# Kernel tuning notes

Measured on AMD Instinct MI355X. Metric: run time of the kernel, lower is better.

Reference implementation:

```python
import jax, jax.numpy as jnp
import numpy as np

B, S, D = 4, 2048, 1024

def setup_inputs() -> dict:
    key = jax.random.key(0)
    ks = jax.random.split(key, 9)
    sc = 1.0 / np.sqrt(D)
    return {
        "x": jax.random.normal(ks[0], (B, S, D), dtype=jnp.float32),
        "Wq": jax.random.normal(ks[1], (D, D), dtype=jnp.float32) * sc,
        "bq": jnp.zeros((D,), dtype=jnp.float32),
        "Wk": jax.random.normal(ks[2], (D, D), dtype=jnp.float32) * sc,
        "bk": jnp.zeros((D,), dtype=jnp.float32),
        "Wv": jax.random.normal(ks[3], (D, D), dtype=jnp.float32) * sc,
        "bv": jnp.zeros((D,), dtype=jnp.float32),
        "Wo": jax.random.normal(ks[4], (D, D), dtype=jnp.float32) * sc,
        "bo": jnp.zeros((D,), dtype=jnp.float32),
    }

def _gaussian_mask(seq_len, dtype):
    # exp(-0.5*((pos - S/2)/(S/4))^2), shape [1,1,S] -> broadcasts over KEY axis
    pos = jnp.arange(seq_len, dtype=dtype)
    center = seq_len / 2
    sigma = seq_len / 4
    m = jnp.exp(-0.5 * ((pos - center) / sigma) ** 2)
    return m[None, None, :]

def reference(x, Wq, bq, Wk, bk, Wv, bv, Wo, bo):
    d = x.shape[-1]
    Q = x @ Wq.T + bq            # [B,S,D]
    K = x @ Wk.T + bk
    V = x @ Wv.T + bv
    scores = jnp.einsum('bqd,bkd->bqk', Q, K) / jnp.sqrt(jnp.asarray(d, x.dtype))
    scores = scores * _gaussian_mask(x.shape[1], x.dtype)
    attn = jax.nn.softmax(scores, axis=-1)
    out = jnp.einsum('bqk,bkd->bqd', attn, V)
    return out @ Wo.T + bo
```

## Files before the change

### kernel.cpp

```cpp
#include <hip/hip_runtime.h>
#include <math.h>

#define SEQ 2048
#define DIM 1024

typedef __attribute__((ext_vector_type(8))) _Float16 half8;
typedef __attribute__((ext_vector_type(4))) float f32x4;

__device__ __forceinline__ unsigned short f2h(float f) {
    union { _Float16 h; unsigned short u; } c; c.h = (_Float16)f;
    return c.u;
}
__device__ __forceinline__ float gmask(int k) {
    float t = ((float)k - 1024.0f) * (1.0f / 512.0f);
    return expf(-0.5f * t * t);
}
__device__ __forceinline__ void glds16(const unsigned short* gp, unsigned short* lp) {
    __builtin_amdgcn_global_load_lds((const __attribute__((address_space(1))) void*)gp,
                                     (__attribute__((address_space(3))) void*)lp, 16, 0, 0);
}

__device__ __forceinline__ void stage64(const unsigned short* __restrict__ g, int ldK,
                                        unsigned short* lds, int wave, int lane) {
    int row = wave * 32 + (lane >> 3);
    int seg = (lane & 7) ^ (lane >> 3);
    const unsigned short* gp = g + (long)row * ldK + seg * 8;
    unsigned short* lp = lds + wave * 2048;
    glds16(gp, lp);
    glds16(gp + 8 * (long)ldK, lp + 512);
    glds16(gp + 16 * (long)ldK, lp + 1024);
    glds16(gp + 24 * (long)ldK, lp + 1536);
}

enum { EPI_QKV = 0, EPI_EXP = 1, EPI_PV = 2, EPI_OUT = 3 };

template <int EPI>
__global__ __launch_bounds__(256, 4) void mfma_gemm(
    const unsigned short* __restrict__ A, const unsigned short* __restrict__ Bm,
    const float* __restrict__ bias,
    float* __restrict__ Cf, unsigned short* __restrict__ Ch,
    int M, int N, int K, float scale, long sA, long sB, long sC)
{
    __shared__ unsigned short As[128 * 64];
    __shared__ unsigned short Bs[128 * 64];

    const int bz = blockIdx.z;
    const int tid = threadIdx.x;
    const int wave = tid >> 6;
    const int lane = tid & 63;
    const int wm = (wave & 1) * 64;
    const int wn = (wave >> 1) * 64;
    const long m0 = (long)blockIdx.y * 128;
    const long n0 = (long)blockIdx.x * 128;
    const int lm = lane & 15;
    const int lk = lane >> 4;

    const unsigned short* pA = A + bz * sA + m0 * K;
    const unsigned short* pB = Bm + bz * sB + n0 * K;

    f32x4 acc[4][4];
#pragma unroll
    for (int i = 0; i < 4; ++i)
#pragma unroll
        for (int j = 0; j < 4; ++j) {
            acc[i][j].x = 0.f; acc[i][j].y = 0.f; acc[i][j].z = 0.f; acc[i][j].w = 0.f;
        }

    int aoff[4][2], boff[4][2];
#pragma unroll
    for (int i = 0; i < 4; ++i)
#pragma unroll
        for (int t = 0; t < 2; ++t) {
            int ar = wm + i * 16 + lm;
            aoff[i][t] = ar * 64 + (((4 * t + lk) ^ (ar & 7)) << 3);
            int br = wn + i * 16 + lm;
            boff[i][t] = br * 64 + (((4 * t + lk) ^ (br & 7)) << 3);
        }

    const int pr = (wave & 1) * 64 + lane;
    const int ph = wave >> 1;
    float psum = 0.f;

    for (int k0 = 0; k0 < K; k0 += 64) {
        stage64(pA + k0, K, As, wave, lane);
        stage64(pB + k0, K, Bs, wave, lane);
        __syncthreads();

        if (EPI == EPI_PV) {
            const unsigned short* rowp = As + pr * 64;
#pragma unroll
            for (int i2 = 0; i2 < 4; ++i2) {
                half8 h = *(const half8*)(rowp + (((2 * i2 + ph) ^ (pr & 7)) << 3));
#pragma unroll
                for (int e = 0; e < 8; ++e) psum += (float)h[e];
            }
        }

#pragma unroll
        for (int t = 0; t < 2; ++t) {
            half8 a[4], b[4];
#pragma unroll
            for (int i = 0; i < 4; ++i) a[i] = *(const half8*)(As + aoff[i][t]);
#pragma unroll
            for (int j = 0; j < 4; ++j) b[j] = *(const half8*)(Bs + boff[j][t]);
#pragma unroll
            for (int i = 0; i < 4; ++i)
#pragma unroll
                for (int j = 0; j < 4; ++j)
                    acc[i][j] = __builtin_amdgcn_mfma_f32_16x16x32_f16(a[i], b[j], acc[i][j], 0, 0, 0);
        }
        __syncthreads();
    }

    float* rsf = (float*)As;
    if (EPI == EPI_PV) {
        rsf[ph * 128 + pr] = psum;
        __syncthreads();
    }

    const long MD = 8388608;
    float* cF = (EPI == EPI_OUT) ? Cf + bz * sC : (float*)nullptr;
    unsigned short* cH = (EPI != EPI_OUT) ? Ch + bz * sC : (unsigned short*)nullptr;

#pragma unroll
    for (int i = 0; i < 4; ++i) {
        long mrow = m0 + wm + i * 16 + lk * 4;
        int lr = wm + i * 16 + lk * 4;
        float inv4[4];
        if (EPI == EPI_PV) {
#pragma unroll
            for (int r = 0; r < 4; ++r)
                inv4[r] = 1.0f / (rsf[lr + r] + rsf[128 + lr + r]);
        }
#pragma unroll
        for (int j = 0; j < 4; ++j) {
            int n = (int)n0 + wn + j * 16 + lm;
            if (EPI == EPI_QKV) {
                int sel = n >> 10;
                int n1 = n & 1023;
                float bs = bias[n];
                if (sel < 2) {
                    unsigned short* dst = cH + (long)sel * MD;
#pragma unroll
                    for (int r = 0; r < 4; ++r)
                        dst[(mrow + r) * (long)DIM + n1] = f2h(acc[i][j][r] + bs);
                } else {
                    long b = mrow >> 11, s = mrow & 2047;
                    long idx = 2 * MD + b * (long)DIM * SEQ + (long)n1 * SEQ + s;
                    unsigned long long pk =
                        (unsigned long long)f2h(acc[i][j].x + bs) |
                        ((unsigned long long)f2h(acc[i][j].y + bs) << 16) |
                        ((unsigned long long)f2h(acc[i][j].z + bs) << 32) |
                        ((unsigned long long)f2h(acc[i][j].w + bs) << 48);
                    *(unsigned long long*)(cH + idx) = pk;
                }
            } else if (EPI == EPI_EXP) {
                float mult = scale * gmask(n);
#pragma unroll
                for (int r = 0; r < 4; ++r)
                    cH[(mrow + r) * (long)N + n] = f2h(expf(acc[i][j][r] * mult));
            } else if (EPI == EPI_PV) {
#pragma unroll
                for (int r = 0; r < 4; ++r)
                    cH[(mrow + r) * (long)N + n] = f2h(acc[i][j][r] * inv4[r]);
            } else {
                float bs = bias[n];
#pragma unroll
                for (int r = 0; r < 4; ++r)
                    cF[(mrow + r) * (long)N + n] = acc[i][j][r] + bs;
            }
        }
    }
}

__global__ __launch_bounds__(256) void prep(
    const float* __restrict__ x,
    const float* __restrict__ Wq, const float* __restrict__ Wk,
    const float* __restrict__ Wv, const float* __restrict__ Wo,
    const float* __restrict__ b0, const float* __restrict__ b1, const float* __restrict__ b2,
    unsigned short* __restrict__ xh, unsigned short* __restrict__ Wp, float* __restrict__ bqkv)
{
    long gid = (long)blockIdx.x * 256 + threadIdx.x;
    if (gid < 3072) {
        int sel = (int)(gid >> 10);
        const float* s = sel == 0 ? b0 : sel == 1 ? b1 : b2;
        bqkv[gid] = s[gid & 1023];
    }
    const long NX = 8388608 / 4;
    const long NW = 1048576 / 4;
    const long total = NX + 4 * NW;
    for (long i = gid; i < total; i += (long)gridDim.x * 256) {
        const float* src; unsigned short* dst; long off;
        if (i < NX) { src = x; dst = xh; off = i; }
        else {
            long wi = i - NX;
            int sel = (int)(wi >> 18);
            src = sel == 0 ? Wq : sel == 1 ? Wk : sel == 2 ? Wv : Wo;
            dst = Wp + ((long)sel << 20);
            off = wi & (NW - 1);
        }
        float4 v = ((const float4*)src)[off];
        unsigned long long p = (unsigned long long)f2h(v.x) | ((unsigned long long)f2h(v.y) << 16) |
                               ((unsigned long long)f2h(v.z) << 32) | ((unsigned long long)f2h(v.w) << 48);
        ((unsigned long long*)dst)[off] = p;
    }
}

extern "C" void kernel_launch(void* const* d_in, const int* in_sizes, int n_in,
                              void* d_out, int out_size, void* d_ws, size_t ws_size,
                              hipStream_t stream)
{
    const float* x  = (const float*)d_in[0];
    const float* Wq = (const float*)d_in[1];
    const float* bq = (const float*)d_in[2];
    const float* Wk = (const float*)d_in[3];
    const float* bk = (const float*)d_in[4];
    const float* Wv = (const float*)d_in[5];
    const float* bv = (const float*)d_in[6];
    const float* Wo = (const float*)d_in[7];
    const float* bo = (const float*)d_in[8];
    float* out = (float*)d_out;

    const long MD = 4L * SEQ * DIM;
    const long WW = (long)DIM * DIM;
    const long SD = (long)SEQ * DIM, SS = (long)SEQ * SEQ;

    unsigned short* xh   = (unsigned short*)d_ws;
    unsigned short* Wp   = xh + MD;
    unsigned short* Woh  = Wp + 3 * WW;
    float* bqkv          = (float*)(Wp + 4 * WW);
    unsigned short* Qh   = (unsigned short*)(bqkv + 4096);
    unsigned short* VT   = Qh + 2 * MD;
    unsigned short* expS = Qh + 3 * MD;
    unsigned short* O1   = xh;

    dim3 blk(256);
    prep<<<4096, blk, 0, stream>>>(x, Wq, Wk, Wv, Wo, bq, bk, bv, xh, Wp, bqkv);

    mfma_gemm<EPI_QKV><<<dim3(3 * DIM / 128, (4 * SEQ) / 128, 1), blk, 0, stream>>>(
        xh, Wp, bqkv, nullptr, Qh, 4 * SEQ, 3 * DIM, DIM, 1.0f, 0, 0, 0);
    mfma_gemm<EPI_EXP><<<dim3(SEQ / 128, SEQ / 128, 4), blk, 0, stream>>>(
        Qh, Qh + MD, nullptr, nullptr, expS, SEQ, SEQ, DIM, 0.03125f, SD, SD, SS);
    mfma_gemm<EPI_PV><<<dim3(DIM / 128, SEQ / 128, 4), blk, 0, stream>>>(
        expS, VT, nullptr, nullptr, O1, SEQ, DIM, SEQ, 1.0f, SS, (long)DIM * SEQ, SD);
    mfma_gemm<EPI_OUT><<<dim3(DIM / 128, (4 * SEQ) / 128, 1), blk, 0, stream>>>(
        O1, Woh, bo, out, nullptr, 4 * SEQ, DIM, DIM, 1.0f, 0, 0, 0);
}
```

Measured before the change: 277.1 us.

## Fuse all stages into one persistent cooperative kernel with grid syncs

Replaces the five separate launches (conversion, QKV GEMM, score-exp GEMM, PV GEMM, output GEMM) with one persistent cooperative kernel. Blocks loop over tiles for each stage and are separated by grid-wide syncs. The aim is to remove per-launch overhead and the idle gaps between dependent kernels. In exchange it adds grid.sync cost, fixes the grid size to the occupancy-limited count, and gives up any overlap the hardware scheduler could find across kernel boundaries.

```diff
diff --git a/kernel.cpp b/kernel.cpp
--- a/kernel.cpp
+++ b/kernel.cpp
@@ -1,5 +1,8 @@
 #include <hip/hip_runtime.h>
+#include <hip/hip_cooperative_groups.h>
 #include <math.h>
+
+namespace cg = cooperative_groups;
 
 #define SEQ 2048
 #define DIM 1024
@@ -35,23 +38,20 @@
 enum { EPI_QKV = 0, EPI_EXP = 1, EPI_PV = 2, EPI_OUT = 3 };
 
 template <int EPI>
-__global__ __launch_bounds__(256, 4) void mfma_gemm(
+__device__ __forceinline__ void gemm_tile(
+    unsigned short* As, unsigned short* Bs, int tid,
+    int tm, int tn, int bz,
     const unsigned short* __restrict__ A, const unsigned short* __restrict__ Bm,
     const float* __restrict__ bias,
     float* __restrict__ Cf, unsigned short* __restrict__ Ch,
-    int M, int N, int K, float scale, long sA, long sB, long sC)
+    int N, int K, float scale, long sA, long sB, long sC)
 {
-    __shared__ unsigned short As[128 * 64];
-    __shared__ unsigned short Bs[128 * 64];
-
-    const int bz = blockIdx.z;
-    const int tid = threadIdx.x;
     const int wave = tid >> 6;
     const int lane = tid & 63;
     const int wm = (wave & 1) * 64;
     const int wn = (wave >> 1) * 64;
-    const long m0 = (long)blockIdx.y * 128;
-    const long n0 = (long)blockIdx.x * 128;
+    const long m0 = (long)tm * 128;
+    const long n0 = (long)tn * 128;
     const int lm = lane & 15;
     const int lk = lane >> 4;
 
@@ -173,37 +173,81 @@
     }
 }
 
-__global__ __launch_bounds__(256) void prep(
+__global__ __launch_bounds__(256, 4) void mega(
     const float* __restrict__ x,
-    const float* __restrict__ Wq, const float* __restrict__ Wk,
-    const float* __restrict__ Wv, const float* __restrict__ Wo,
-    const float* __restrict__ b0, const float* __restrict__ b1, const float* __restrict__ b2,
-    unsigned short* __restrict__ xh, unsigned short* __restrict__ Wp, float* __restrict__ bqkv)
+    const float* __restrict__ Wq, const float* __restrict__ bq,
+    const float* __restrict__ Wk, const float* __restrict__ bk,
+    const float* __restrict__ Wv, const float* __restrict__ bv,
+    const float* __restrict__ Wo, const float* __restrict__ bo,
+    void* __restrict__ ws, float* __restrict__ out)
 {
-    long gid = (long)blockIdx.x * 256 + threadIdx.x;
-    if (gid < 3072) {
-        int sel = (int)(gid >> 10);
-        const float* s = sel == 0 ? b0 : sel == 1 ? b1 : b2;
-        bqkv[gid] = s[gid & 1023];
-    }
-    const long NX = 8388608 / 4;
-    const long NW = 1048576 / 4;
-    const long total = NX + 4 * NW;
-    for (long i = gid; i < total; i += (long)gridDim.x * 256) {
-        const float* src; unsigned short* dst; long off;
-        if (i < NX) { src = x; dst = xh; off = i; }
-        else {
-            long wi = i - NX;
-            int sel = (int)(wi >> 18);
-            src = sel == 0 ? Wq : sel == 1 ? Wk : sel == 2 ? Wv : Wo;
-            dst = Wp + ((long)sel << 20);
-            off = wi & (NW - 1);
-        }
-        float4 v = ((const float4*)src)[off];
-        unsigned long long p = (unsigned long long)f2h(v.x) | ((unsigned long long)f2h(v.y) << 16) |
-                               ((unsigned long long)f2h(v.z) << 32) | ((unsigned long long)f2h(v.w) << 48);
-        ((unsigned long long*)dst)[off] = p;
-    }
+    __shared__ unsigned short As[128 * 64];
+    __shared__ unsigned short Bs[128 * 64];
+
+    const long MD = 8388608;
+    const long WW = 1048576;
+    const long SD = (long)SEQ * DIM, SS = (long)SEQ * SEQ;
+
+    unsigned short* xh   = (unsigned short*)ws;
+    unsigned short* Wp   = xh + MD;
+    unsigned short* Woh  = Wp + 3 * WW;
+    float* bqkv          = (float*)(Wp + 4 * WW);
+    unsigned short* Qh   = (unsigned short*)(bqkv + 4096);
+    unsigned short* VT   = Qh + 2 * MD;
+    unsigned short* expS = Qh + 3 * MD;
+    unsigned short* O1   = xh;
+
+    cg::grid_group grid = cg::this_grid();
+    const int tid = threadIdx.x;
+    const int bid = blockIdx.x;
+    const int nblk = gridDim.x;
+
+    {
+        long gid = (long)bid * 256 + tid;
+        if (gid < 3072) {
+            int sel = (int)(gid >> 10);
+            const float* s = sel == 0 ? bq : sel == 1 ? bk : bv;
+            bqkv[gid] = s[gid & 1023];
+        }
+        const long NX = MD / 4;
+        const long NW = WW / 4;
+        const long total = NX + 4 * NW;
+        for (long i = gid; i < total; i += (long)nblk * 256) {
+            const float* src; unsigned short* dst; long off;
+            if (i < NX) { src = x; dst = xh; off = i; }
+            else {
+                long wi = i - NX;
+                int sel = (int)(wi >> 18);
+                src = sel == 0 ? Wq : sel == 1 ? Wk : sel == 2 ? Wv : Wo;
+                dst = Wp + ((long)sel << 20);
+                off = wi & (NW - 1);
+            }
+            float4 v = ((const float4*)src)[off];
+            unsigned long long p = (unsigned long long)f2h(v.x) | ((unsigned long long)f2h(v.y) << 16) |
+                                   ((unsigned long long)f2h(v.z) << 32) | ((unsigned long long)f2h(v.w) << 48);
+            ((unsigned long long*)dst)[off] = p;
+        }
+    }
+    grid.sync();
+
+    for (int t = bid; t < 1536; t += nblk)
+        gemm_tile<EPI_QKV>(As, Bs, tid, t & 63, t >> 6, 0,
+                           xh, Wp, bqkv, nullptr, Qh, 3 * DIM, DIM, 1.0f, 0, 0, 0);
+    grid.sync();
+
+    for (int t = bid; t < 1024; t += nblk)
+        gemm_tile<EPI_EXP>(As, Bs, tid, (t >> 4) & 15, t & 15, t >> 8,
+                           Qh, Qh + MD, nullptr, nullptr, expS, SEQ, DIM, 0.03125f, SD, SD, SS);
+    grid.sync();
+
+    for (int t = bid; t < 512; t += nblk)
+        gemm_tile<EPI_PV>(As, Bs, tid, (t >> 3) & 15, t & 7, t >> 7,
+                          expS, VT, nullptr, nullptr, O1, DIM, SEQ, 1.0f, SS, (long)DIM * SEQ, SD);
+    grid.sync();
+
+    for (int t = bid; t < 512; t += nblk)
+        gemm_tile<EPI_OUT>(As, Bs, tid, t >> 3, t & 7, 0,
+                           O1, Woh, bo, out, nullptr, DIM, DIM, 1.0f, 0, 0, 0);
 }
 
 extern "C" void kernel_launch(void* const* d_in, const int* in_sizes, int n_in,
@@ -220,29 +264,15 @@
     const float* Wo = (const float*)d_in[7];
     const float* bo = (const float*)d_in[8];
     float* out = (float*)d_out;
-
-    const long MD = 4L * SEQ * DIM;
-    const long WW = (long)DIM * DIM;
-    const long SD = (long)SEQ * DIM, SS = (long)SEQ * SEQ;
-
-    unsigned short* xh   = (unsigned short*)d_ws;
-    unsigned short* Wp   = xh + MD;
-    unsigned short* Woh  = Wp + 3 * WW;
-    float* bqkv          = (float*)(Wp + 4 * WW);
-    unsigned short* Qh   = (unsigned short*)(bqkv + 4096);
-    unsigned short* VT   = Qh + 2 * MD;
-    unsigned short* expS = Qh + 3 * MD;
-    unsigned short* O1   = xh;
-
-    dim3 blk(256);
-    prep<<<4096, blk, 0, stream>>>(x, Wq, Wk, Wv, Wo, bq, bk, bv, xh, Wp, bqkv);
-
-    mfma_gemm<EPI_QKV><<<dim3(3 * DIM / 128, (4 * SEQ) / 128, 1), blk, 0, stream>>>(
-        xh, Wp, bqkv, nullptr, Qh, 4 * SEQ, 3 * DIM, DIM, 1.0f, 0, 0, 0);
-    mfma_gemm<EPI_EXP><<<dim3(SEQ / 128, SEQ / 128, 4), blk, 0, stream>>>(
-        Qh, Qh + MD, nullptr, nullptr, expS, SEQ, SEQ, DIM, 0.03125f, SD, SD, SS);
-    mfma_gemm<EPI_PV><<<dim3(DIM / 128, SEQ / 128, 4), blk, 0, stream>>>(
-        expS, VT, nullptr, nullptr, O1, SEQ, DIM, SEQ, 1.0f, SS, (long)DIM * SEQ, SD);
-    mfma_gemm<EPI_OUT><<<dim3(DIM / 128, (4 * SEQ) / 128, 1), blk, 0, stream>>>(
-        O1, Woh, bo, out, nullptr, 4 * SEQ, DIM, DIM, 1.0f, 0, 0, 0);
-}
+    void* ws = d_ws;
+
+    int maxb = 2;
+    (void)hipOccupancyMaxActiveBlocksPerMultiprocessor(&maxb, (const void*)mega, 256, 0);
+    if (maxb < 1) maxb = 1;
+    if (maxb > 4) maxb = 4;
+    int nblk = 256 * maxb;
+
+    void* args[] = { (void*)&x, (void*)&Wq, (void*)&bq, (void*)&Wk, (void*)&bk,
+                     (void*)&Wv, (void*)&bv, (void*)&Wo, (void*)&bo, (void*)&ws, (void*)&out };
+    hipLaunchCooperativeKernel((const void*)mega, dim3(nblk), dim3(256), args, 0, stream);
+}
```

Result: slower. 574.1 us (+107.2%).
